# Kernel optimization log

Hardware: AMD Instinct MI355X
Metric: run time of the kernel (lower is better)

## Reference

```python
import jax, jax.numpy as jnp
import numpy as np
import math

B, S, D, H = 4, 2048, 1024, 16
DK = D // H

def setup_inputs() -> dict:
    key = jax.random.key(0)
    ks = jax.random.split(key, 11)
    mk = lambda k, shape: jax.random.normal(k, shape, dtype=jnp.float32)
    inp = {
        'query': mk(ks[0], (B, S, D)),
        'key':   mk(ks[1], (B, S, D)),
        'value': mk(ks[2], (B, S, D)),
        'Wq': mk(ks[3], (D, D)) * 0.02, 'bq': jnp.zeros((D,), jnp.float32),
        'Wk': mk(ks[4], (D, D)) * 0.02, 'bk': jnp.zeros((D,), jnp.float32),
        'Wv': mk(ks[5], (D, D)) * 0.02, 'bv': jnp.zeros((D,), jnp.float32),
        'Wo': mk(ks[6], (D, D)) * 0.02, 'bo': jnp.zeros((D,), jnp.float32),
    }
    return inp

def reference(query, key, value, Wq, bq, Wk, bk, Wv, bv, Wo, bo):
    b, s, d = query.shape
    scale = 1.0 / math.sqrt(DK)
    def proj(x, W, bias):
        # nn.Linear: x @ W.T + b, then split heads -> [b, h, s, dk]
        return (x @ W.T + bias).reshape(b, s, H, DK).transpose(0, 2, 1, 3)
    q = proj(query, Wq, bq)
    k = proj(key, Wk, bk)
    v = proj(value, Wv, bv)
    scores = jnp.einsum('bhqd,bhkd->bhqk', q, k) * scale  # [b,h,s,s]
    attn = jax.nn.softmax(scores, axis=-1)
    # dropout is identity in eval/reference mode
    x = jnp.einsum('bhqk,bhkd->bhqd', attn, v)
    x = x.transpose(0, 2, 1, 3).reshape(b, s, d)
    return x @ Wo.T + bo
```

## Files before the change

### kernel.cpp

```cpp
#include <hip/hip_runtime.h>
#include <stdint.h>

#define DEV static __device__ __forceinline__

typedef __bf16 bf16_t;
typedef bf16_t bf16x8 __attribute__((ext_vector_type(8)));
typedef bf16_t bf16x4 __attribute__((ext_vector_type(4)));
typedef float f32x4 __attribute__((ext_vector_type(4)));

static constexpr int Bc = 4, Sc = 2048, Dc = 1024, Hc = 16, DKc = 64;
static constexpr int Mrows = Bc * Sc;

DEV unsigned short f2bf(float f) {
  unsigned int u = __float_as_uint(f);
  u += 0x7fffu + ((u >> 16) & 1u);
  return (unsigned short)(u >> 16);
}

DEV float fexp2(float x) {
#if __has_builtin(__builtin_amdgcn_exp2f)
  return __builtin_amdgcn_exp2f(x);
#else
  return exp2f(x);
#endif
}

#if __has_builtin(__builtin_amdgcn_mfma_f32_16x16x16_bf16)
DEV f32x4 mfma16(bf16x4 a, bf16x4 b, f32x4 c) {
  return __builtin_amdgcn_mfma_f32_16x16x16_bf16(a, b, c, 0, 0, 0);
}
#elif __has_builtin(__builtin_amdgcn_mfma_f32_16x16x16bf16_1k)
typedef short s16x4 __attribute__((ext_vector_type(4)));
DEV f32x4 mfma16(bf16x4 a, bf16x4 b, f32x4 c) {
  union U { bf16x4 h; s16x4 s; };
  U ua, ub; ua.h = a; ub.h = b;
  return __builtin_amdgcn_mfma_f32_16x16x16bf16_1k(ua.s, ub.s, c, 0, 0, 0);
}
#else
DEV f32x4 mfma16(bf16x4 a, bf16x4 b, f32x4 c) {
  asm("v_mfma_f32_16x16x16_bf16 %0, %1, %2, %0" : "+v"(c) : "v"(a), "v"(b));
  return c;
}
#endif

DEV void gload_lds16(const void* g, void* l) {
  __builtin_amdgcn_global_load_lds(
      (const __attribute__((address_space(1))) void*)g,
      (__attribute__((address_space(3))) void*)l, 16, 0, 0);
}

__global__ void __launch_bounds__(256) cvt_bf16_seg_kernel(
    const float* __restrict__ s0, const float* __restrict__ s1,
    const float* __restrict__ s2, const float* __restrict__ s3,
    unsigned short* __restrict__ out, int lg) {
  int i = blockIdx.x * blockDim.x + threadIdx.x;
  int seg = i >> lg, j = i & ((1 << lg) - 1);
  const float* src = seg == 0 ? s0 : seg == 1 ? s1 : seg == 2 ? s2 : s3;
  float4 v = reinterpret_cast<const float4*>(src)[j];
  ushort4 o;
  o.x = f2bf(v.x); o.y = f2bf(v.y); o.z = f2bf(v.z); o.w = f2bf(v.w);
  reinterpret_cast<ushort4*>(out)[i] = o;
}

template <bool QKV>
__global__ void __launch_bounds__(256) gemm_dbuf_kernel(
    const unsigned short* __restrict__ A0, const unsigned short* __restrict__ A1,
    const unsigned short* __restrict__ A2,
    const unsigned short* __restrict__ W0, const unsigned short* __restrict__ W1,
    const unsigned short* __restrict__ W2,
    const float* __restrict__ b0, const float* __restrict__ b1,
    const float* __restrict__ b2,
    void* __restrict__ C0, void* __restrict__ C1, void* __restrict__ C2,
    int M, int N, int K, float scale0) {
  __shared__ unsigned short lA[3][128 * 32];
  __shared__ unsigned short lB[3][128 * 32];
  const int t = threadIdx.x;
  const int wv = t >> 6, ln = t & 63;
  const int l15 = ln & 15, lhi = ln >> 4;

  const unsigned short* A; const unsigned short* W;
  const float* bias; void* Cout; float scale; int mode;
  if (QKV) {
    const int z = blockIdx.z;
    A = z == 0 ? A0 : z == 1 ? A1 : A2;
    W = z == 0 ? W0 : z == 1 ? W1 : W2;
    bias = z == 0 ? b0 : z == 1 ? b1 : b2;
    Cout = z == 0 ? C0 : z == 1 ? C1 : C2;
    scale = z == 0 ? scale0 : 1.0f;
    mode = z == 2 ? 2 : 1;
  } else {
    A = A0; W = W0; bias = b0; Cout = C0; scale = scale0; mode = 0;
  }

  const int nwg = gridDim.x * gridDim.y;
  const int hw = blockIdx.y * gridDim.x + blockIdx.x;
  const int chunk = nwg >> 3;
  const int swzid = (hw & 7) * chunk + (hw >> 3);
  const int m0 = (swzid / gridDim.x) * 128, n0 = (swzid % gridDim.x) * 128;
  const int wr = wv >> 1, wc = wv & 1;
  const int swzR = (l15 & 3) << 4;

  const int rowA = t >> 2;
  const int colS = ((t & 3) ^ (rowA & 3)) * 8;
  const unsigned short* aS = A + (size_t)(m0 + rowA) * K + colS;
  const unsigned short* wS = W + (size_t)(n0 + rowA) * K + colS;
  const size_t rstep = (size_t)64 * K;
  const int d0 = t * 16, d1 = 4096 + t * 16;

  f32x4 acc[4][4] = {};

#define GSTAGE(bi, k0_)                                        \
  do {                                                         \
    gload_lds16(aS + (k0_), (char*)lA[bi] + d0);               \
    gload_lds16(aS + rstep + (k0_), (char*)lA[bi] + d1);       \
    gload_lds16(wS + (k0_), (char*)lB[bi] + d0);               \
    gload_lds16(wS + rstep + (k0_), (char*)lB[bi] + d1);       \
  } while (0)

  GSTAGE(0, 0);
  GSTAGE(1, 32);

  const int NK = K >> 5;
  int cur = 0, stg = 2;
  for (int tk = 0; tk < NK; ++tk) {
    if (tk == NK - 1)
      asm volatile("s_waitcnt vmcnt(0)" ::: "memory");
    else
      asm volatile("s_waitcnt vmcnt(4)" ::: "memory");
    __builtin_amdgcn_s_barrier();
    __builtin_amdgcn_sched_barrier(0);

    if (tk + 2 < NK) GSTAGE(stg, (tk + 2) * 32);

    bf16x8 af[4], bfr[4];
#pragma unroll
    for (int i = 0; i < 4; ++i)
      af[i] = *reinterpret_cast<const bf16x8*>(
          (char*)lA[cur] + (((wr * 64 + i * 16 + l15) * 64 + lhi * 16) ^ swzR));
#pragma unroll
    for (int j = 0; j < 4; ++j)
      bfr[j] = *reinterpret_cast<const bf16x8*>(
          (char*)lB[cur] + (((wc * 64 + j * 16 + l15) * 64 + lhi * 16) ^ swzR));
#pragma unroll
    for (int i = 0; i < 4; ++i)
#pragma unroll
      for (int j = 0; j < 4; ++j)
        acc[i][j] = __builtin_amdgcn_mfma_f32_16x16x32_bf16(af[i], bfr[j], acc[i][j], 0, 0, 0);

    cur = cur == 2 ? 0 : cur + 1;
    stg = stg == 2 ? 0 : stg + 1;
  }
#undef GSTAGE

#pragma unroll
  for (int i = 0; i < 4; ++i)
#pragma unroll
    for (int j = 0; j < 4; ++j) {
      int n = n0 + wc * 64 + j * 16 + l15;
      float bv = bias[n];
      if (QKV && mode == 2) {
        int mb = m0 + wr * 64 + i * 16 + lhi * 4;
        int sl = mb & (Sc - 1);
        int pl = (sl & ~60) | ((sl & 48) >> 2) | ((sl & 12) << 2);
        ushort4 ov;
        ov.x = f2bf((acc[i][j][0] + bv) * scale);
        ov.y = f2bf((acc[i][j][1] + bv) * scale);
        ov.z = f2bf((acc[i][j][2] + bv) * scale);
        ov.w = f2bf((acc[i][j][3] + bv) * scale);
        *reinterpret_cast<ushort4*>((unsigned short*)Cout +
            ((size_t)(mb >> 11) * Dc + n) * Sc + pl) = ov;
      } else {
#pragma unroll
        for (int jj = 0; jj < 4; ++jj) {
          int m = m0 + wr * 64 + i * 16 + lhi * 4 + jj;
          float v = (acc[i][j][jj] + bv) * scale;
          if (QKV)
            ((unsigned short*)Cout)[(size_t)m * N + n] = f2bf(v);
          else
            ((float*)Cout)[(size_t)m * N + n] = v;
        }
      }
    }
}

__global__ void __launch_bounds__(512, 4) attn_kernel(
    const unsigned short* __restrict__ Q, const unsigned short* __restrict__ Kk,
    const unsigned short* __restrict__ Vt, unsigned short* __restrict__ X) {
  __shared__ unsigned short lK[3][64 * 64];
  __shared__ unsigned short lVT[3][64 * 64];
  const int t = threadIdx.x;
  const int wv = t >> 6, ln = t & 63;
  const int l15 = ln & 15, lhi = ln >> 4;
  const int q0 = blockIdx.x * 128;
  const int h = blockIdx.y, b = blockIdx.z;
  const size_t base = (size_t)b * Sc * Dc;
  const int hoff = h * DKc;

  bf16x8 qf[2];
  {
    const unsigned short* qp = Q + base + (size_t)(q0 + wv * 16 + l15) * Dc + hoff + lhi * 8;
    qf[0] = *reinterpret_cast<const bf16x8*>(qp);
    qf[1] = *reinterpret_cast<const bf16x8*>(qp + 32);
  }

  const int e0 = t * 8;
  const int r0 = e0 >> 6, c0 = (e0 & 63) ^ ((r0 & 7) << 3);
  const unsigned short* kS0 = Kk + base + (size_t)r0 * Dc + hoff + c0;
  const unsigned short* vS0 = Vt + ((size_t)b * Dc + hoff + r0) * Sc + c0;

  float mrow = -1e30f;
  f32x4 xacc[4] = {};
  f32x4 lsum = {};
  const int swzK = (l15 & 7) << 4;

  bf16x4 ones4;
#pragma unroll
  for (int i = 0; i < 4; ++i) ones4[i] = (bf16_t)1.0f;

#define STAGE(bi, kv0_)                                                    \
  do {                                                                     \
    gload_lds16(kS0 + (size_t)(kv0_)*Dc, (char*)lK[bi] + e0 * 2);          \
    gload_lds16(vS0 + (kv0_), (char*)lVT[bi] + e0 * 2);                    \
  } while (0)

  STAGE(0, 0);
  STAGE(1, 64);

  const int NT = Sc / 64;
  int cur = 0, stg = 2;
  for (int tt = 0; tt < NT; ++tt) {
    if (tt == NT - 1)
      asm volatile("s_waitcnt vmcnt(0)" ::: "memory");
    else
      asm volatile("s_waitcnt vmcnt(2)" ::: "memory");
    __builtin_amdgcn_s_barrier();
    __builtin_amdgcn_sched_barrier(0);

    if (tt + 2 < NT) STAGE(stg, (tt + 2) * 64);

    const unsigned short* K_ = lK[cur];
    const unsigned short* VT_ = lVT[cur];

    f32x4 sacc[4];
#pragma unroll
    for (int ct = 0; ct < 4; ++ct) {
      f32x4 z = {};
#pragma unroll
      for (int kk = 0; kk < 2; ++kk) {
        bf16x8 kf = *reinterpret_cast<const bf16x8*>(
            (const char*)K_ + (((ct * 16 + l15) * 128 + kk * 64 + lhi * 16) ^ swzK));
        z = __builtin_amdgcn_mfma_f32_16x16x32_bf16(kf, qf[kk], z, 0, 0, 0);
      }
      sacc[ct] = z;
    }

    float mt = fmaxf(fmaxf(sacc[0][0], sacc[0][1]), fmaxf(sacc[0][2], sacc[0][3]));
#pragma unroll
    for (int ct = 1; ct < 4; ++ct)
      mt = fmaxf(mt,
          fmaxf(fmaxf(sacc[ct][0], sacc[ct][1]), fmaxf(sacc[ct][2], sacc[ct][3])));

    if (__any(mt > mrow + 8.0f)) {
      float mtr = fmaxf(mt, __shfl_xor(mt, 16));
      mtr = fmaxf(mtr, __shfl_xor(mtr, 32));
      float mnew = fmaxf(mrow, mtr);
      float corr = fexp2(mrow - mnew);
      mrow = mnew;
#pragma unroll
      for (int jj = 0; jj < 4; ++jj) {
        float cO = __shfl(corr, lhi * 4 + jj);
        lsum[jj] *= cO;
#pragma unroll
        for (int dt = 0; dt < 4; ++dt) xacc[dt][jj] *= cO;
      }
    }

    bf16x4 pa[4];
#pragma unroll
    for (int ct = 0; ct < 4; ++ct)
#pragma unroll
      for (int jj = 0; jj < 4; ++jj)
        pa[ct][jj] = (bf16_t)fexp2(sacc[ct][jj] - mrow);

#pragma unroll
    for (int ct = 0; ct < 4; ++ct) lsum = mfma16(pa[ct], ones4, lsum);

#pragma unroll
    for (int dt = 0; dt < 4; ++dt) {
#pragma unroll
      for (int sel = 0; sel < 2; ++sel) {
        bf16x8 vb2 = *reinterpret_cast<const bf16x8*>(
            (const char*)VT_ + (((dt * 16 + l15) * 128 + lhi * 32 + sel * 16) ^ swzK));
        bf16x4 vlo = __builtin_shufflevector(vb2, vb2, 0, 1, 2, 3);
        bf16x4 vhi = __builtin_shufflevector(vb2, vb2, 4, 5, 6, 7);
        xacc[dt] = mfma16(pa[2 * sel + 0], vlo, xacc[dt]);
        xacc[dt] = mfma16(pa[2 * sel + 1], vhi, xacc[dt]);
      }
    }

    cur = cur == 2 ? 0 : cur + 1;
    stg = stg == 2 ? 0 : stg + 1;
  }
#undef STAGE

  float iO[4];
#pragma unroll
  for (int jj = 0; jj < 4; ++jj) iO[jj] = 1.0f / lsum[jj];

  unsigned short* xp = X + base + (size_t)(q0 + wv * 16) * Dc + hoff;
#pragma unroll
  for (int dt = 0; dt < 4; ++dt)
#pragma unroll
    for (int jj = 0; jj < 4; ++jj) {
      int r = lhi * 4 + jj;
      xp[(size_t)r * Dc + dt * 16 + l15] = f2bf(xacc[dt][jj] * iO[jj]);
    }
}

extern "C" void kernel_launch(void* const* d_in, const int* in_sizes, int n_in,
                              void* d_out, int out_size, void* d_ws, size_t ws_size,
                              hipStream_t stream) {
  const float* query = (const float*)d_in[0];
  const float* key   = (const float*)d_in[1];
  const float* value = (const float*)d_in[2];
  const float* Wq = (const float*)d_in[3];
  const float* bq = (const float*)d_in[4];
  const float* Wk = (const float*)d_in[5];
  const float* bk = (const float*)d_in[6];
  const float* Wv = (const float*)d_in[7];
  const float* bv = (const float*)d_in[8];
  const float* Wo = (const float*)d_in[9];
  const float* bo = (const float*)d_in[10];

  const size_t NBS = (size_t)Mrows * Dc;
  const size_t NW  = (size_t)Dc * Dc;
  unsigned short* bQin = (unsigned short*)d_ws;
  unsigned short* bKin = bQin + NBS;
  unsigned short* bVin = bKin + NBS;
  unsigned short* bWq  = bVin + NBS;
  unsigned short* bWk  = bWq + NW;
  unsigned short* bWv  = bWk + NW;
  unsigned short* bWo  = bWv + NW;
  unsigned short* Qp   = bWo + NW;
  unsigned short* Kp   = Qp + NBS;
  unsigned short* Vtp  = Kp + NBS;
  unsigned short* Xp   = Vtp + NBS;

  cvt_bf16_seg_kernel<<<(int)(3 * NBS / 1024), 256, 0, stream>>>(
      query, key, value, value, bQin, 21);
  cvt_bf16_seg_kernel<<<(int)(4 * NW / 1024), 256, 0, stream>>>(
      Wq, Wk, Wv, Wo, bWq, 18);

  gemm_dbuf_kernel<true><<<dim3(Dc / 128, Mrows / 128, 3), 256, 0, stream>>>(
      bQin, bKin, bVin, bWq, bWk, bWv, bq, bk, bv, Qp, Kp, Vtp,
      Mrows, Dc, Dc, 0.125f * 1.44269504088896340736f);

  attn_kernel<<<dim3(Sc / 128, Hc, Bc), 512, 0, stream>>>(Qp, Kp, Vtp, Xp);

  gemm_dbuf_kernel<false><<<dim3(Dc / 128, Mrows / 128, 1), 256, 0, stream>>>(
      Xp, nullptr, nullptr, bWo, nullptr, nullptr, bo, nullptr, nullptr,
      d_out, nullptr, nullptr, Mrows, Dc, Dc, 1.0f);
}
```

Baseline: 232.7 us.

## Double-buffer 128-wide KV tiles with folded max offset and MFMA priority

Replaces the triple-buffered 64-row KV pipeline with a double-buffered 128-row tile per iteration, so there is one barrier per 128 keys instead of per 64. The running max is folded into the QK accumulator initial value (nm), so the exp needs no per-element subtraction. s_setprio is raised around the MFMA regions to favour matrix work over other waves' loads. The trade-off is prefetch depth dropping from two tiles ahead to one, with a full vmcnt(0) wait each iteration, plus more live registers for the larger score tile.

Result: no change. 228.8 us (-1.7%).

```diff
diff --git a/kernel.cpp b/kernel.cpp
--- a/kernel.cpp
+++ b/kernel.cpp
@@ -186,8 +186,8 @@
 __global__ void __launch_bounds__(512, 4) attn_kernel(
     const unsigned short* __restrict__ Q, const unsigned short* __restrict__ Kk,
     const unsigned short* __restrict__ Vt, unsigned short* __restrict__ X) {
-  __shared__ unsigned short lK[3][64 * 64];
-  __shared__ unsigned short lVT[3][64 * 64];
+  __shared__ unsigned short lK[2][128 * 64];
+  __shared__ unsigned short lVT[2][64 * 128];
   const int t = threadIdx.x;
   const int wv = t >> 6, ln = t & 63;
   const int l15 = ln & 15, lhi = ln >> 4;
@@ -203,12 +203,14 @@
     qf[1] = *reinterpret_cast<const bf16x8*>(qp + 32);
   }
 
-  const int e0 = t * 8;
-  const int r0 = e0 >> 6, c0 = (e0 & 63) ^ ((r0 & 7) << 3);
-  const unsigned short* kS0 = Kk + base + (size_t)r0 * Dc + hoff + c0;
-  const unsigned short* vS0 = Vt + ((size_t)b * Dc + hoff + r0) * Sc + c0;
-
-  float mrow = -1e30f;
+  const int kvr = t >> 3;
+  const int kcol = ((t & 7) * 8) ^ ((kvr & 7) << 3);
+  const unsigned short* kS = Kk + base + (size_t)kvr * Dc + hoff + kcol;
+  const int vdk = t >> 4;
+  const int vkv = ((t & 15) * 8) ^ ((vdk & 7) << 3);
+  const unsigned short* vS = Vt + ((size_t)b * Dc + hoff + vdk) * Sc + vkv;
+
+  float nm = 0.f;
   f32x4 xacc[4] = {};
   f32x4 lsum = {};
   const int swzK = (l15 & 7) << 4;
@@ -217,55 +219,62 @@
 #pragma unroll
   for (int i = 0; i < 4; ++i) ones4[i] = (bf16_t)1.0f;
 
-#define STAGE(bi, kv0_)                                                    \
-  do {                                                                     \
-    gload_lds16(kS0 + (size_t)(kv0_)*Dc, (char*)lK[bi] + e0 * 2);          \
-    gload_lds16(vS0 + (kv0_), (char*)lVT[bi] + e0 * 2);                    \
+#define DSTAGE(bi, kv0_)                                                        \
+  do {                                                                          \
+    gload_lds16(kS + (size_t)(kv0_)*Dc, (char*)lK[bi] + t * 16);                \
+    gload_lds16(kS + (size_t)((kv0_) + 64) * Dc, (char*)lK[bi] + 8192 + t * 16);\
+    gload_lds16(vS + (kv0_), (char*)lVT[bi] + t * 16);                          \
+    gload_lds16(vS + (size_t)32 * Sc + (kv0_), (char*)lVT[bi] + 8192 + t * 16); \
   } while (0)
 
-  STAGE(0, 0);
-  STAGE(1, 64);
-
-  const int NT = Sc / 64;
-  int cur = 0, stg = 2;
-  for (int tt = 0; tt < NT; ++tt) {
-    if (tt == NT - 1)
-      asm volatile("s_waitcnt vmcnt(0)" ::: "memory");
-    else
-      asm volatile("s_waitcnt vmcnt(2)" ::: "memory");
-    __builtin_amdgcn_s_barrier();
-    __builtin_amdgcn_sched_barrier(0);
-
-    if (tt + 2 < NT) STAGE(stg, (tt + 2) * 64);
-
-    const unsigned short* K_ = lK[cur];
-    const unsigned short* VT_ = lVT[cur];
-
-    f32x4 sacc[4];
-#pragma unroll
-    for (int ct = 0; ct < 4; ++ct) {
-      f32x4 z = {};
-#pragma unroll
-      for (int kk = 0; kk < 2; ++kk) {
-        bf16x8 kf = *reinterpret_cast<const bf16x8*>(
-            (const char*)K_ + (((ct * 16 + l15) * 128 + kk * 64 + lhi * 16) ^ swzK));
-        z = __builtin_amdgcn_mfma_f32_16x16x32_bf16(kf, qf[kk], z, 0, 0, 0);
+  DSTAGE(0, 0);
+  asm volatile("s_waitcnt vmcnt(0)" ::: "memory");
+  __builtin_amdgcn_s_barrier();
+  __builtin_amdgcn_sched_barrier(0);
+
+  const int NT2 = Sc / 128;
+  for (int tt = 0; tt < NT2; ++tt) {
+    const int cur = tt & 1;
+    if (tt + 1 < NT2) DSTAGE(cur ^ 1, (tt + 1) * 128);
+
+    const char* K_ = (const char*)lK[cur];
+    const char* VT_ = (const char*)lVT[cur];
+
+    f32x4 nm4 = {nm, nm, nm, nm};
+    f32x4 sacc[2][4];
+    __builtin_amdgcn_s_setprio(1);
+#pragma unroll
+    for (int s64 = 0; s64 < 2; ++s64)
+#pragma unroll
+      for (int ct = 0; ct < 4; ++ct) {
+        f32x4 z = nm4;
+#pragma unroll
+        for (int kk = 0; kk < 2; ++kk) {
+          bf16x8 kf = *reinterpret_cast<const bf16x8*>(
+              K_ + (((s64 * 64 + ct * 16 + l15) * 128 + kk * 64 + lhi * 16) ^ swzK));
+          z = __builtin_amdgcn_mfma_f32_16x16x32_bf16(kf, qf[kk], z, 0, 0, 0);
+        }
+        sacc[s64][ct] = z;
       }
-      sacc[ct] = z;
-    }
-
-    float mt = fmaxf(fmaxf(sacc[0][0], sacc[0][1]), fmaxf(sacc[0][2], sacc[0][3]));
-#pragma unroll
-    for (int ct = 1; ct < 4; ++ct)
-      mt = fmaxf(mt,
-          fmaxf(fmaxf(sacc[ct][0], sacc[ct][1]), fmaxf(sacc[ct][2], sacc[ct][3])));
-
-    if (__any(mt > mrow + 8.0f)) {
+    __builtin_amdgcn_s_setprio(0);
+
+    float m0a = fmaxf(fmaxf(sacc[0][0][0], sacc[0][0][1]), fmaxf(sacc[0][0][2], sacc[0][0][3]));
+    float m0b = fmaxf(fmaxf(sacc[0][1][0], sacc[0][1][1]), fmaxf(sacc[0][1][2], sacc[0][1][3]));
+    float m0c = fmaxf(fmaxf(sacc[0][2][0], sacc[0][2][1]), fmaxf(sacc[0][2][2], sacc[0][2][3]));
+    float m0d = fmaxf(fmaxf(sacc[0][3][0], sacc[0][3][1]), fmaxf(sacc[0][3][2], sacc[0][3][3]));
+    float m1a = fmaxf(fmaxf(sacc[1][0][0], sacc[1][0][1]), fmaxf(sacc[1][0][2], sacc[1][0][3]));
+    float m1b = fmaxf(fmaxf(sacc[1][1][0], sacc[1][1][1]), fmaxf(sacc[1][1][2], sacc[1][1][3]));
+    float m1c = fmaxf(fmaxf(sacc[1][2][0], sacc[1][2][1]), fmaxf(sacc[1][2][2], sacc[1][2][3]));
+    float m1d = fmaxf(fmaxf(sacc[1][3][0], sacc[1][3][1]), fmaxf(sacc[1][3][2], sacc[1][3][3]));
+    float mt = fmaxf(fmaxf(fmaxf(m0a, m0b), fmaxf(m0c, m0d)),
+                     fmaxf(fmaxf(m1a, m1b), fmaxf(m1c, m1d)));
+
+    if (__any(mt > 8.0f)) {
       float mtr = fmaxf(mt, __shfl_xor(mt, 16));
       mtr = fmaxf(mtr, __shfl_xor(mtr, 32));
-      float mnew = fmaxf(mrow, mtr);
-      float corr = fexp2(mrow - mnew);
-      mrow = mnew;
+      float mte = fmaxf(mtr, 0.f);
+      float corr = fexp2(-mte);
+      nm -= mte;
 #pragma unroll
       for (int jj = 0; jj < 4; ++jj) {
         float cO = __shfl(corr, lhi * 4 + jj);
@@ -273,35 +282,45 @@
 #pragma unroll
         for (int dt = 0; dt < 4; ++dt) xacc[dt][jj] *= cO;
       }
+#pragma unroll
+      for (int s64 = 0; s64 < 2; ++s64)
+#pragma unroll
+        for (int ct = 0; ct < 4; ++ct)
+#pragma unroll
+          for (int jj = 0; jj < 4; ++jj) sacc[s64][ct][jj] -= mte;
     }
 
-    bf16x4 pa[4];
-#pragma unroll
-    for (int ct = 0; ct < 4; ++ct)
-#pragma unroll
-      for (int jj = 0; jj < 4; ++jj)
-        pa[ct][jj] = (bf16_t)fexp2(sacc[ct][jj] - mrow);
-
-#pragma unroll
-    for (int ct = 0; ct < 4; ++ct) lsum = mfma16(pa[ct], ones4, lsum);
-
-#pragma unroll
-    for (int dt = 0; dt < 4; ++dt) {
-#pragma unroll
-      for (int sel = 0; sel < 2; ++sel) {
-        bf16x8 vb2 = *reinterpret_cast<const bf16x8*>(
-            (const char*)VT_ + (((dt * 16 + l15) * 128 + lhi * 32 + sel * 16) ^ swzK));
-        bf16x4 vlo = __builtin_shufflevector(vb2, vb2, 0, 1, 2, 3);
-        bf16x4 vhi = __builtin_shufflevector(vb2, vb2, 4, 5, 6, 7);
-        xacc[dt] = mfma16(pa[2 * sel + 0], vlo, xacc[dt]);
-        xacc[dt] = mfma16(pa[2 * sel + 1], vhi, xacc[dt]);
+    __builtin_amdgcn_s_setprio(1);
+#pragma unroll
+    for (int s64 = 0; s64 < 2; ++s64) {
+      bf16x4 pa[4];
+#pragma unroll
+      for (int ct = 0; ct < 4; ++ct)
+#pragma unroll
+        for (int jj = 0; jj < 4; ++jj)
+          pa[ct][jj] = (bf16_t)fexp2(sacc[s64][ct][jj]);
+#pragma unroll
+      for (int ct = 0; ct < 4; ++ct) lsum = mfma16(pa[ct], ones4, lsum);
+#pragma unroll
+      for (int dt = 0; dt < 4; ++dt) {
+#pragma unroll
+        for (int sel = 0; sel < 2; ++sel) {
+          bf16x8 vb2 = *reinterpret_cast<const bf16x8*>(
+              VT_ + (((dt * 16 + l15) * 256 + s64 * 128 + lhi * 32 + sel * 16) ^ swzK));
+          bf16x4 vlo = __builtin_shufflevector(vb2, vb2, 0, 1, 2, 3);
+          bf16x4 vhi = __builtin_shufflevector(vb2, vb2, 4, 5, 6, 7);
+          xacc[dt] = mfma16(pa[2 * sel + 0], vlo, xacc[dt]);
+          xacc[dt] = mfma16(pa[2 * sel + 1], vhi, xacc[dt]);
+        }
       }
     }
-
-    cur = cur == 2 ? 0 : cur + 1;
-    stg = stg == 2 ? 0 : stg + 1;
+    __builtin_amdgcn_s_setprio(0);
+
+    asm volatile("s_waitcnt vmcnt(0)" ::: "memory");
+    __builtin_amdgcn_s_barrier();
+    __builtin_amdgcn_sched_barrier(0);
   }
-#undef STAGE
+#undef DSTAGE
 
   float iO[4];
 #pragma unroll
```
